# Optimization experiments

Measured on AMD Instinct MI355X. Metric: run time of the kernel, lower is better.

The kernel has to match this reference:

```python
import jax, jax.numpy as jnp
import numpy as np

N_NODES = 100000
N_EDGES = 3200000
D_FEAT = 128
K_ADJ = 3


def setup_inputs() -> dict:
    key = jax.random.key(0)
    k1, k2, k3, k4 = jax.random.split(key, 4)
    x = jax.random.normal(k1, (N_NODES, D_FEAT), dtype=jnp.float32)
    adj_rows = jax.random.randint(k2, (K_ADJ, N_EDGES), 0, N_NODES, dtype=jnp.int32)
    adj_cols = jax.random.randint(k3, (K_ADJ, N_EDGES), 0, N_NODES, dtype=jnp.int32)
    adj_vals = jax.random.uniform(k4, (K_ADJ, N_EDGES), dtype=jnp.float32)
    return {"x": x, "adj_rows": adj_rows, "adj_cols": adj_cols, "adj_vals": adj_vals, "idx": 1}


def reference(x, adj_rows, adj_cols, adj_vals, idx):
    # torch.spmm(adjs[idx], x): out[r] = sum_{e: rows[e]==r} vals[e] * x[cols[e]]
    rows = adj_rows[idx]
    cols = adj_cols[idx]
    vals = adj_vals[idx]
    gathered = x[cols] * vals[:, None]  # [nnz, F]
    out = jax.ops.segment_sum(gathered, rows, num_segments=N_NODES)  # [N, F]
    return out
```

## Files before the change

kernel.cpp:

```cpp
#include <hip/hip_runtime.h>

#define N_NODES 100000
#define N_EDGES 3200000
#define D_FEAT  128

#define RPB 128
#define NB ((N_NODES + RPB - 1) / RPB)
#define P3_THREADS 512
#define P3_EPT 32
#define P3_TILE (P3_THREADS * P3_EPT)
#define P3_GRID ((N_EDGES + P3_TILE - 1) / P3_TILE)

#define NS 25
#define NCELL (RPB * NS)
#define CAP 4608

#define CVT_BLOCKS 2048
#define HIST_BLOCKS 256


__device__ inline unsigned bf16rne(float f) {
    unsigned u = __float_as_uint(f);
    u += 0x7fffu + ((u >> 16) & 1u);
    return u >> 16;
}
__device__ inline unsigned pack2(float lo, float hi) {
    return bf16rne(lo) | (bf16rne(hi) << 16);
}

__global__ __launch_bounds__(256) void cvt_bhist_kernel(
    const float* __restrict__ x, uint4* __restrict__ xb,
    const int* __restrict__ adj_rows, const int* __restrict__ idx_p,
    int* __restrict__ bhist)
{
    __shared__ int lh[NB];
    if (blockIdx.x < CVT_BLOCKS) {
        const int total = N_NODES * D_FEAT / 8;
        for (int i = blockIdx.x * 256 + threadIdx.x; i < total;
             i += CVT_BLOCKS * 256) {
            const float4 a = reinterpret_cast<const float4*>(x)[2 * i];
            const float4 b = reinterpret_cast<const float4*>(x)[2 * i + 1];
            uint4 o;
            o.x = pack2(a.x, a.y);
            o.y = pack2(a.z, a.w);
            o.z = pack2(b.x, b.y);
            o.w = pack2(b.z, b.w);
            xb[i] = o;
        }
    } else {
        for (int i = threadIdx.x; i < NB; i += 256) lh[i] = 0;
        __syncthreads();
        const long long idx = (long long)idx_p[0];
        const int* rows = adj_rows + idx * (long long)N_EDGES;
        for (int e = (blockIdx.x - CVT_BLOCKS) * 256 + threadIdx.x;
             e < N_EDGES; e += HIST_BLOCKS * 256)
            atomicAdd(&lh[rows[e] >> 7], 1);
        __syncthreads();
        for (int i = threadIdx.x; i < NB; i += 256)
            if (lh[i]) atomicAdd(&bhist[i], lh[i]);
    }
}

__global__ __launch_bounds__(1024) void bscan_kernel(
    const int* __restrict__ bhist, int* __restrict__ bptr,
    int* __restrict__ bcursor)
{
    __shared__ int lds[1024];
    const int t = threadIdx.x;
    const int v = (t < NB) ? bhist[t] : 0;
    lds[t] = v;
    __syncthreads();
    for (int off = 1; off < 1024; off <<= 1) {
        int u = (t >= off) ? lds[t - off] : 0;
        __syncthreads();
        lds[t] += u;
        __syncthreads();
    }
    if (t < NB) {
        const int excl = lds[t] - v;
        bptr[t]    = excl;
        bcursor[t] = excl;
    }
    if (t == NB - 1) bptr[NB] = lds[t];
}

__global__ __launch_bounds__(P3_THREADS) void partition_kernel(
    const int* __restrict__ adj_rows, const int* __restrict__ adj_cols,
    const float* __restrict__ adj_vals, const int* __restrict__ idx_p,
    int* __restrict__ bcursor, int2* __restrict__ pairs)
{
    __shared__ int lcnt[NB];
    __shared__ int lbase[NB];
    const long long idx = (long long)idx_p[0];
    const int*   rows = adj_rows + idx * (long long)N_EDGES;
    const int*   cols = adj_cols + idx * (long long)N_EDGES;
    const float* vals = adj_vals + idx * (long long)N_EDGES;

    const int tile = blockIdx.x * P3_TILE;
    for (int i = threadIdx.x; i < NB; i += P3_THREADS) lcnt[i] = 0;
    __syncthreads();

    int rc[P3_EPT];
#pragma unroll
    for (int k = 0; k < P3_EPT; ++k) {
        const int e = tile + k * P3_THREADS + (int)threadIdx.x;
        rc[k] = (e < N_EDGES) ? rows[e] : -1;
        if (rc[k] >= 0) atomicAdd(&lcnt[rc[k] >> 7], 1);
    }
    __syncthreads();

    for (int i = threadIdx.x; i < NB; i += P3_THREADS) {
        const int c = lcnt[i];
        lbase[i] = c ? atomicAdd(&bcursor[i], c) : 0;
        lcnt[i]  = 0;
    }
    __syncthreads();

#pragma unroll
    for (int k = 0; k < P3_EPT; ++k) {
        const int r = rc[k];
        if (r >= 0) {
            const int e = tile + k * P3_THREADS + (int)threadIdx.x;
            const int b = r >> 7;
            const int pos = lbase[b] + atomicAdd(&lcnt[b], 1);
            pairs[pos] = make_int2(((r & (RPB - 1)) << 24) | cols[e],
                                   __float_as_int(vals[e]));
        }
    }
}

__global__ __launch_bounds__(1024) void sort_spmm_kernel(
    const uint4* __restrict__ xb, const int* __restrict__ bptr,
    const int2* __restrict__ pairs, float* __restrict__ out)
{
    __shared__ int2 staged[CAP];
    __shared__ int  cellptr[NCELL];
    __shared__ int  rs[RPB + 1];
    __shared__ int  scan[1024];
    const int b    = blockIdx.x;
    const int t    = (int)threadIdx.x;
    const int base = bptr[b];
    const int n    = bptr[b + 1] - base;

    for (int i = t; i < NCELL; i += 1024) cellptr[i] = 0;
    __syncthreads();

    for (int i = t; i < n; i += 1024) {
        const int2 p = pairs[base + i];
        const int row = ((unsigned)p.x) >> 24;
        const int col = p.x & 0xFFFFFF;
        atomicAdd(&cellptr[row * NS + (col >> 12)], 1);
    }
    __syncthreads();

    const int i0 = t * 4;
    int v0 = 0, v1 = 0, v2 = 0, v3 = 0;
    if (i0 + 0 < NCELL) v0 = cellptr[i0 + 0];
    if (i0 + 1 < NCELL) v1 = cellptr[i0 + 1];
    if (i0 + 2 < NCELL) v2 = cellptr[i0 + 2];
    if (i0 + 3 < NCELL) v3 = cellptr[i0 + 3];
    const int s = v0 + v1 + v2 + v3;
    scan[t] = s;
    __syncthreads();
    for (int off = 1; off < 1024; off <<= 1) {
        int u = (t >= off) ? scan[t - off] : 0;
        __syncthreads();
        scan[t] += u;
        __syncthreads();
    }
    int run = scan[t] - s;
    if (i0 + 0 < NCELL) { cellptr[i0 + 0] = run; run += v0; }
    if (i0 + 1 < NCELL) { cellptr[i0 + 1] = run; run += v1; }
    if (i0 + 2 < NCELL) { cellptr[i0 + 2] = run; run += v2; }
    if (i0 + 3 < NCELL) { cellptr[i0 + 3] = run; run += v3; }
    __syncthreads();

    if (t < RPB) rs[t] = cellptr[t * NS];
    if (t == 0)  rs[RPB] = n;
    __syncthreads();

    for (int i = t; i < n; i += 1024) {
        const int2 p = pairs[base + i];
        const int row = ((unsigned)p.x) >> 24;
        const int col = p.x & 0xFFFFFF;
        const int pos = atomicAdd(&cellptr[row * NS + (col >> 12)], 1);
        if (pos < CAP) staged[pos] = p;
    }
    __syncthreads();

    const int w    = t >> 6;
    const int lane = t & 63;
    const int g    = lane >> 4;
    const int sl   = lane & 15;
    const int grp  = w * 4 + g;

    for (int k = 0; k < 2; ++k) {
        const int r   = grp + 64 * k;
        const int row = b * RPB + r;
        if (row >= N_NODES) break;
        const int s0 = rs[r];
        const int e0 = rs[r + 1];

        float4 a0 = make_float4(0.f, 0.f, 0.f, 0.f);
        float4 a1 = make_float4(0.f, 0.f, 0.f, 0.f);
        for (int j = s0; j < e0; ++j) {
            const int2  p   = staged[j];
            const int   col = p.x & 0xFFFFFF;
            const float vj  = __int_as_float(p.y);
            const uint4 wv  = xb[(size_t)col * (D_FEAT / 8) + sl];
            a0.x += vj * __uint_as_float(wv.x << 16);
            a0.y += vj * __uint_as_float(wv.x & 0xffff0000u);
            a0.z += vj * __uint_as_float(wv.y << 16);
            a0.w += vj * __uint_as_float(wv.y & 0xffff0000u);
            a1.x += vj * __uint_as_float(wv.z << 16);
            a1.y += vj * __uint_as_float(wv.z & 0xffff0000u);
            a1.z += vj * __uint_as_float(wv.w << 16);
            a1.w += vj * __uint_as_float(wv.w & 0xffff0000u);
        }
        float* op = out + (size_t)row * D_FEAT + sl * 8;
        *reinterpret_cast<float4*>(op)     = a0;
        *reinterpret_cast<float4*>(op + 4) = a1;
    }
}

__global__ __launch_bounds__(256) void spmm_atomic_kernel(
    const float* __restrict__ x,
    const int*   __restrict__ adj_rows,
    const int*   __restrict__ adj_cols,
    const float* __restrict__ adj_vals,
    const int*   __restrict__ idx_p,
    float*       __restrict__ out)
{
    const long long idx = (long long)idx_p[0];
    const int*   rows = adj_rows + idx * (long long)N_EDGES;
    const int*   cols = adj_cols + idx * (long long)N_EDGES;
    const float* vals = adj_vals + idx * (long long)N_EDGES;

    long long tt = (long long)blockIdx.x * blockDim.x + threadIdx.x;
    long long e  = tt >> 5;
    int       f4 = (int)(tt & 31);
    if (e >= N_EDGES) return;

    const int   r = rows[e];
    const int   c = cols[e];
    const float v = vals[e];
    const float4 xv =
        *reinterpret_cast<const float4*>(x + (long long)c * D_FEAT + f4 * 4);
    float* o = out + (long long)r * D_FEAT + f4 * 4;
    unsafeAtomicAdd(o + 0, v * xv.x);
    unsafeAtomicAdd(o + 1, v * xv.y);
    unsafeAtomicAdd(o + 2, v * xv.z);
    unsafeAtomicAdd(o + 3, v * xv.w);
}

extern "C" void kernel_launch(void* const* d_in, const int* in_sizes, int n_in,
                              void* d_out, int out_size, void* d_ws, size_t ws_size,
                              hipStream_t stream) {
    const float* x        = (const float*)d_in[0];
    const int*   adj_rows = (const int*)  d_in[1];
    const int*   adj_cols = (const int*)  d_in[2];
    const float* adj_vals = (const float*)d_in[3];
    const int*   idx_p    = (const int*)  d_in[4];
    float*       out      = (float*)d_out;

    const size_t n_meta_raw = (size_t)NB * 3 + 1;
    const size_t n_meta     = (n_meta_raw + 3) & ~(size_t)3;
    const size_t need       = (n_meta + (size_t)2 * N_EDGES) * 4
                            + (size_t)N_NODES * D_FEAT * 2;

    if (ws_size < need) {
        hipMemsetAsync(out, 0, (size_t)out_size * sizeof(float), stream);
        const long long total_threads = (long long)N_EDGES * 32;
        const int block = 256;
        const long long grid = (total_threads + block - 1) / block;
        spmm_atomic_kernel<<<(dim3)(unsigned)grid, block, 0, stream>>>(
            x, adj_rows, adj_cols, adj_vals, idx_p, out);
        return;
    }

    int*   bhist   = (int*)d_ws;
    int*   bptr    = bhist + NB;
    int*   bcursor = bptr + (NB + 1);
    int2*  pairs   = (int2*)((int*)d_ws + n_meta);
    uint4* xb      = (uint4*)((int*)d_ws + n_meta + (size_t)2 * N_EDGES);

    hipMemsetAsync(bhist, 0, (size_t)NB * sizeof(int), stream);

    cvt_bhist_kernel<<<CVT_BLOCKS + HIST_BLOCKS, 256, 0, stream>>>(
        x, xb, adj_rows, idx_p, bhist);
    bscan_kernel<<<1, 1024, 0, stream>>>(bhist, bptr, bcursor);
    partition_kernel<<<P3_GRID, P3_THREADS, 0, stream>>>(
        adj_rows, adj_cols, adj_vals, idx_p, bcursor, pairs);
    sort_spmm_kernel<<<NB, 1024, 0, stream>>>(xb, bptr, pairs, out);
}
```

Measured before the change: 222.8 us.

## Fold bucket scan into partition kernel, reorder hist blocks, add nontemporal memory ops

The separate single-block scan kernel is removed. Every partition block now redundantly scans the bucket histogram into shared memory, and block 0 writes bptr to global. bcursor now starts at zero via a widened memset and is offset by the local scan result. Histogram blocks are moved first and increased in number relative to the conversion blocks. Nontemporal loads are used for pairs and nontemporal stores for out. The aim is to save a kernel launch and serial gap at the cost of duplicated scan work per block.

```diff
diff --git a/kernel.cpp b/kernel.cpp
--- a/kernel.cpp
+++ b/kernel.cpp
@@ -15,8 +15,11 @@
 #define NCELL (RPB * NS)
 #define CAP 4608
 
-#define CVT_BLOCKS 2048
-#define HIST_BLOCKS 256
+#define HIST_BLOCKS 768
+#define CVT_BLOCKS 1536
+
+typedef int   nt_i2 __attribute__((ext_vector_type(2)));
+typedef float nt_f4 __attribute__((ext_vector_type(4)));
 
 
 __device__ inline unsigned bf16rne(float f) {
@@ -34,9 +37,20 @@
     int* __restrict__ bhist)
 {
     __shared__ int lh[NB];
-    if (blockIdx.x < CVT_BLOCKS) {
+    if (blockIdx.x < HIST_BLOCKS) {
+        for (int i = threadIdx.x; i < NB; i += 256) lh[i] = 0;
+        __syncthreads();
+        const long long idx = (long long)idx_p[0];
+        const int* rows = adj_rows + idx * (long long)N_EDGES;
+        for (int e = blockIdx.x * 256 + threadIdx.x; e < N_EDGES;
+             e += HIST_BLOCKS * 256)
+            atomicAdd(&lh[rows[e] >> 7], 1);
+        __syncthreads();
+        for (int i = threadIdx.x; i < NB; i += 256)
+            if (lh[i]) atomicAdd(&bhist[i], lh[i]);
+    } else {
         const int total = N_NODES * D_FEAT / 8;
-        for (int i = blockIdx.x * 256 + threadIdx.x; i < total;
+        for (int i = (blockIdx.x - HIST_BLOCKS) * 256 + threadIdx.x; i < total;
              i += CVT_BLOCKS * 256) {
             const float4 a = reinterpret_cast<const float4*>(x)[2 * i];
             const float4 b = reinterpret_cast<const float4*>(x)[2 * i + 1];
@@ -47,69 +61,61 @@
             o.w = pack2(b.z, b.w);
             xb[i] = o;
         }
-    } else {
-        for (int i = threadIdx.x; i < NB; i += 256) lh[i] = 0;
-        __syncthreads();
-        const long long idx = (long long)idx_p[0];
-        const int* rows = adj_rows + idx * (long long)N_EDGES;
-        for (int e = (blockIdx.x - CVT_BLOCKS) * 256 + threadIdx.x;
-             e < N_EDGES; e += HIST_BLOCKS * 256)
-            atomicAdd(&lh[rows[e] >> 7], 1);
-        __syncthreads();
-        for (int i = threadIdx.x; i < NB; i += 256)
-            if (lh[i]) atomicAdd(&bhist[i], lh[i]);
-    }
-}
-
-__global__ __launch_bounds__(1024) void bscan_kernel(
-    const int* __restrict__ bhist, int* __restrict__ bptr,
-    int* __restrict__ bcursor)
-{
-    __shared__ int lds[1024];
-    const int t = threadIdx.x;
-    const int v = (t < NB) ? bhist[t] : 0;
-    lds[t] = v;
-    __syncthreads();
-    for (int off = 1; off < 1024; off <<= 1) {
-        int u = (t >= off) ? lds[t - off] : 0;
-        __syncthreads();
-        lds[t] += u;
-        __syncthreads();
-    }
-    if (t < NB) {
-        const int excl = lds[t] - v;
-        bptr[t]    = excl;
-        bcursor[t] = excl;
-    }
-    if (t == NB - 1) bptr[NB] = lds[t];
+    }
 }
 
 __global__ __launch_bounds__(P3_THREADS) void partition_kernel(
     const int* __restrict__ adj_rows, const int* __restrict__ adj_cols,
     const float* __restrict__ adj_vals, const int* __restrict__ idx_p,
-    int* __restrict__ bcursor, int2* __restrict__ pairs)
+    const int* __restrict__ bhist, int* __restrict__ bcursor,
+    int* __restrict__ bptr, int2* __restrict__ pairs)
 {
     __shared__ int lcnt[NB];
     __shared__ int lbase[NB];
+    __shared__ int lbptr[NB];
+    __shared__ int sscan[P3_THREADS];
+    const int t = (int)threadIdx.x;
+
+    const int e0 = 2 * t, e1 = 2 * t + 1;
+    const int v0 = (e0 < NB) ? bhist[e0] : 0;
+    const int v1 = (e1 < NB) ? bhist[e1] : 0;
+    const int ss = v0 + v1;
+    sscan[t] = ss;
+    if (t < NB) lcnt[t] = 0;
+    if (t + P3_THREADS < NB) lcnt[t + P3_THREADS] = 0;
+    __syncthreads();
+    for (int off = 1; off < P3_THREADS; off <<= 1) {
+        int u = (t >= off) ? sscan[t - off] : 0;
+        __syncthreads();
+        sscan[t] += u;
+        __syncthreads();
+    }
+    const int pre = sscan[t] - ss;
+    if (e0 < NB) lbptr[e0] = pre;
+    if (e1 < NB) lbptr[e1] = pre + v0;
+    if (blockIdx.x == 0) {
+        if (e0 < NB) bptr[e0] = pre;
+        if (e1 < NB) bptr[e1] = pre + v0;
+        if (t == P3_THREADS - 1) bptr[NB] = sscan[t];
+    }
+    __syncthreads();
+
     const long long idx = (long long)idx_p[0];
     const int*   rows = adj_rows + idx * (long long)N_EDGES;
     const int*   cols = adj_cols + idx * (long long)N_EDGES;
     const float* vals = adj_vals + idx * (long long)N_EDGES;
-
     const int tile = blockIdx.x * P3_TILE;
-    for (int i = threadIdx.x; i < NB; i += P3_THREADS) lcnt[i] = 0;
-    __syncthreads();
 
     int rc[P3_EPT];
 #pragma unroll
     for (int k = 0; k < P3_EPT; ++k) {
-        const int e = tile + k * P3_THREADS + (int)threadIdx.x;
+        const int e = tile + k * P3_THREADS + t;
         rc[k] = (e < N_EDGES) ? rows[e] : -1;
         if (rc[k] >= 0) atomicAdd(&lcnt[rc[k] >> 7], 1);
     }
     __syncthreads();
 
-    for (int i = threadIdx.x; i < NB; i += P3_THREADS) {
+    for (int i = t; i < NB; i += P3_THREADS) {
         const int c = lcnt[i];
         lbase[i] = c ? atomicAdd(&bcursor[i], c) : 0;
         lcnt[i]  = 0;
@@ -120,9 +126,9 @@
     for (int k = 0; k < P3_EPT; ++k) {
         const int r = rc[k];
         if (r >= 0) {
-            const int e = tile + k * P3_THREADS + (int)threadIdx.x;
+            const int e = tile + k * P3_THREADS + t;
             const int b = r >> 7;
-            const int pos = lbase[b] + atomicAdd(&lcnt[b], 1);
+            const int pos = lbptr[b] + lbase[b] + atomicAdd(&lcnt[b], 1);
             pairs[pos] = make_int2(((r & (RPB - 1)) << 24) | cols[e],
                                    __float_as_int(vals[e]));
         }
@@ -180,11 +186,13 @@
     __syncthreads();
 
     for (int i = t; i < n; i += 1024) {
-        const int2 p = pairs[base + i];
-        const int row = ((unsigned)p.x) >> 24;
-        const int col = p.x & 0xFFFFFF;
+        const nt_i2 pr = __builtin_nontemporal_load(
+            reinterpret_cast<const nt_i2*>(pairs + base + i));
+        const int w0 = pr[0];
+        const int row = ((unsigned)w0) >> 24;
+        const int col = w0 & 0xFFFFFF;
         const int pos = atomicAdd(&cellptr[row * NS + (col >> 12)], 1);
-        if (pos < CAP) staged[pos] = p;
+        if (pos < CAP) staged[pos] = make_int2(w0, pr[1]);
     }
     __syncthreads();
 
@@ -218,8 +226,10 @@
             a1.w += vj * __uint_as_float(wv.w & 0xffff0000u);
         }
         float* op = out + (size_t)row * D_FEAT + sl * 8;
-        *reinterpret_cast<float4*>(op)     = a0;
-        *reinterpret_cast<float4*>(op + 4) = a1;
+        nt_f4 o0 = {a0.x, a0.y, a0.z, a0.w};
+        nt_f4 o1 = {a1.x, a1.y, a1.z, a1.w};
+        __builtin_nontemporal_store(o0, reinterpret_cast<nt_f4*>(op));
+        __builtin_nontemporal_store(o1, reinterpret_cast<nt_f4*>(op) + 1);
     }
 }
 
@@ -279,17 +289,16 @@
     }
 
     int*   bhist   = (int*)d_ws;
-    int*   bptr    = bhist + NB;
-    int*   bcursor = bptr + (NB + 1);
+    int*   bcursor = bhist + NB;
+    int*   bptr    = bcursor + NB;
     int2*  pairs   = (int2*)((int*)d_ws + n_meta);
     uint4* xb      = (uint4*)((int*)d_ws + n_meta + (size_t)2 * N_EDGES);
 
-    hipMemsetAsync(bhist, 0, (size_t)NB * sizeof(int), stream);
-
-    cvt_bhist_kernel<<<CVT_BLOCKS + HIST_BLOCKS, 256, 0, stream>>>(
+    hipMemsetAsync(d_ws, 0, (size_t)(2 * NB) * sizeof(int), stream);
+
+    cvt_bhist_kernel<<<HIST_BLOCKS + CVT_BLOCKS, 256, 0, stream>>>(
         x, xb, adj_rows, idx_p, bhist);
-    bscan_kernel<<<1, 1024, 0, stream>>>(bhist, bptr, bcursor);
     partition_kernel<<<P3_GRID, P3_THREADS, 0, stream>>>(
-        adj_rows, adj_cols, adj_vals, idx_p, bcursor, pairs);
+        adj_rows, adj_cols, adj_vals, idx_p, bhist, bcursor, bptr, pairs);
     sort_spmm_kernel<<<NB, 1024, 0, stream>>>(xb, bptr, pairs, out);
 }
```

Result: no change. 221.0 us (-0.8%).
